# Optimization experiments

Hardware: AMD Instinct MI355X
Metric: run time of the kernel (lower is better)

## Reference

```python
import jax, jax.numpy as jnp
import numpy as np

B, R, T, D = 16, 1024, 512, 1024
H = 1024  # hidden_dim

def setup_inputs() -> dict:
    key = jax.random.key(0)
    ks = jax.random.split(key, 8)
    s_in = 1.0 / np.sqrt(D)
    s_comb = 1.0 / np.sqrt(3 * D)
    return {
        "region_feats": jax.random.normal(ks[0], (B, R, D), jnp.float32),
        "query_embs": jax.random.normal(ks[1], (B, T, D), jnp.float32),
        "Wr": jax.random.normal(ks[2], (D, H), jnp.float32) * s_in,
        "br": jnp.zeros((H,), jnp.float32),
        "Wq": jax.random.normal(ks[3], (D, H), jnp.float32) * s_in,
        "bq": jnp.zeros((H,), jnp.float32),
        "Ws": jax.random.normal(ks[4], (3 * D, 1), jnp.float32) * s_comb,
        "bs": jnp.zeros((1,), jnp.float32),
    }

def reference(region_feats, query_embs, Wr, br, Wq, bq, Ws, bs):
    # Dense projections
    R_proj = region_feats @ Wr + br            # [B,R,H]
    Q_proj = query_embs @ Wq + bq              # [B,T,H]
    # Unscaled cross-attention scores
    scores = jnp.einsum('brd,btd->brt', R_proj, Q_proj)  # [B,R,T]
    attn = jax.nn.softmax(scores, axis=-1)
    # Attend over RAW query embeddings (as in source)
    attended = jnp.einsum('brt,btd->brd', attn, query_embs)  # [B,R,D]
    combined = jnp.concatenate(
        [region_feats, attended, region_feats * attended], axis=-1)  # [B,R,3D]
    out = combined @ Ws + bs                    # [B,R,1]
    return jnp.squeeze(out, axis=-1)            # [B,R]
```

## Files before the change

### kernel.cpp

```cpp
#include <hip/hip_runtime.h>


#define BD 16
#define RD 1024
#define TD 512
#define DD 1024
#define BR (BD * RD)

typedef _Float16 half8 __attribute__((ext_vector_type(8)));
typedef _Float16 half4 __attribute__((ext_vector_type(4)));
typedef float floatx4 __attribute__((ext_vector_type(4)));

__device__ __forceinline__ float wave_sum(float v) {
#pragma unroll
  for (int off = 32; off > 0; off >>= 1) v += __shfl_down(v, off);
  return v;
}

template <bool FUSED>
__global__ __launch_bounds__(512, 4) void gemm_pipe(
    const _Float16* __restrict__ A, const _Float16* __restrict__ B0,
    const _Float16* __restrict__ B1, _Float16* __restrict__ C,
    float* __restrict__ Ms, float* __restrict__ Ls, float* __restrict__ Hs,
    const float* __restrict__ cvec, const _Float16* __restrict__ wsh,
    int N, int K, long sA, long sB, long sC, int remap) {
  constexpr int TT = FUSED ? 3 : 2;
  __shared__ __align__(16) _Float16 lds[2 * TT * 4096];
  __shared__ __align__(16) _Float16 wlds[FUSED ? 2048 : 16];

  const int lin = blockIdx.x + gridDim.x * (blockIdx.y + gridDim.y * blockIdx.z);
  int b, mt, nt;
  if (remap == 2) {
    const int s = lin & 7, u = lin >> 3;
    b = 2 * s + (u >> 5);
    const int t = u & 31;
    mt = t >> 2; nt = t & 3;
  } else if (remap == 1) {
    const int s = lin & 7, u = lin >> 3;
    b = 0;
    mt = s * 8 + (u >> 3); nt = u & 7;
  } else {
    b = blockIdx.z; mt = blockIdx.y; nt = blockIdx.x;
  }
  const int m0 = mt * 128, n0 = nt * 128;
  A += (long)b * sA;
  B0 += (long)b * sB;
  if (FUSED) B1 += (long)b * sB;

  const int tid = threadIdx.x, lane = tid & 63, w = tid >> 6;
  const int wr = w >> 1, wc = w & 1;

  const int lrow = lane >> 2;
  const int slot = lane & 3;
  const int scol = (slot ^ ((lrow >> 1) & 3)) * 8;
  const int srow = 16 * w + lrow;
  const _Float16* gA = A + (long)(m0 + srow) * K + scol;
  const _Float16* gP = B0 + (long)(n0 + srow) * K + scol;
  const _Float16* gQ = FUSED ? B1 + (long)(n0 + srow) * K + scol : nullptr;
  const int wofs = srow * 32 + slot * 8;

  if (FUSED && tid < 256) *(int4*)&wlds[tid * 8] = *(const int4*)&wsh[tid * 8];

  const int NK = K / 32;
  int4 pA, pP, pQ;
  pA = *(const int4*)gA;
  pP = *(const int4*)gP;
  if (FUSED) pQ = *(const int4*)gQ;
  *(int4*)&lds[wofs] = pA;
  *(int4*)&lds[4096 + wofs] = pP;
  if (FUSED) *(int4*)&lds[8192 + wofs] = pQ;
  if (NK > 1) {
    pA = *(const int4*)(gA + 32);
    pP = *(const int4*)(gP + 32);
    if (FUSED) pQ = *(const int4*)(gQ + 32);
  }
  __syncthreads();

  floatx4 accS[2][4] = {};
  floatx4 accH[2][4] = {};
  const int fr = lane & 15, g = lane >> 4;
  const int fs = (g ^ ((fr >> 1) & 3)) * 8;

  for (int kt = 0; kt < NK; ++kt) {
    const int cur = (kt & 1) * TT * 4096;
    const int nxt = ((kt + 1) & 1) * TT * 4096;
    if (kt + 1 < NK) {
      *(int4*)&lds[nxt + wofs] = pA;
      *(int4*)&lds[nxt + 4096 + wofs] = pP;
      if (FUSED) *(int4*)&lds[nxt + 8192 + wofs] = pQ;
    }
    if (kt + 2 < NK) {
      const long go = (long)(kt + 2) * 32;
      pA = *(const int4*)(gA + go);
      pP = *(const int4*)(gP + go);
      if (FUSED) pQ = *(const int4*)(gQ + go);
    }
    half8 af[2], bp[4], bq[4], w1f, w2f;
#pragma unroll
    for (int i = 0; i < 2; ++i)
      af[i] = *(const half8*)&lds[cur + (32 * wr + 16 * i + fr) * 32 + fs];
#pragma unroll
    for (int j = 0; j < 4; ++j)
      bp[j] = *(const half8*)&lds[cur + 4096 + (64 * wc + 16 * j + fr) * 32 + fs];
    if (FUSED) {
#pragma unroll
      for (int j = 0; j < 4; ++j)
        bq[j] = *(const half8*)&lds[cur + 8192 + (64 * wc + 16 * j + fr) * 32 + fs];
      w1f = *(const half8*)&wlds[kt * 32 + g * 8];
      w2f = *(const half8*)&wlds[1024 + kt * 32 + g * 8];
    }
#pragma unroll
    for (int i = 0; i < 2; ++i)
#pragma unroll
      for (int j = 0; j < 4; ++j)
        accS[i][j] = __builtin_amdgcn_mfma_f32_16x16x32_f16(af[i], bp[j], accS[i][j], 0, 0, 0);
    if (FUSED) {
#pragma unroll
      for (int i = 0; i < 2; ++i) af[i] = w1f + af[i] * w2f;
#pragma unroll
      for (int i = 0; i < 2; ++i)
#pragma unroll
        for (int j = 0; j < 4; ++j)
          accH[i][j] = __builtin_amdgcn_mfma_f32_16x16x32_f16(af[i], bq[j], accH[i][j], 0, 0, 0);
    }
    __syncthreads();
  }

  const int cr = g * 4, cc = fr;
  if (!FUSED) {
    _Float16* Cw = C + (long)b * sC;
#pragma unroll
    for (int i = 0; i < 2; ++i)
#pragma unroll
      for (int r = 0; r < 4; ++r)
#pragma unroll
        for (int j = 0; j < 4; ++j)
          Cw[(long)(m0 + 32 * wr + 16 * i + cr + r) * N + n0 + 64 * wc + 16 * j + cc] =
              (_Float16)accS[i][j][r];
  } else {
    float cv[4];
#pragma unroll
    for (int j = 0; j < 4; ++j)
      cv[j] = cvec[(long)b * TD + n0 + 64 * wc + 16 * j + cc];
    const int chunk = nt * 2 + wc;
    const long rowBase = (long)b * RD + m0 + 32 * wr + cr;
#pragma unroll
    for (int i = 0; i < 2; ++i) {
#pragma unroll
      for (int r = 0; r < 4; ++r) {
        float mx = -1e30f;
#pragma unroll
        for (int j = 0; j < 4; ++j) mx = fmaxf(mx, accS[i][j][r] + cv[j]);
        mx = fmaxf(mx, __shfl_xor(mx, 1));
        mx = fmaxf(mx, __shfl_xor(mx, 2));
        mx = fmaxf(mx, __shfl_xor(mx, 4));
        mx = fmaxf(mx, __shfl_xor(mx, 8));
        float l = 0.f, hs = 0.f;
#pragma unroll
        for (int j = 0; j < 4; ++j) {
          const float e = __expf(accS[i][j][r] + cv[j] - mx);
          l += e;
          hs += e * accH[i][j][r];
        }
        l += __shfl_xor(l, 1); hs += __shfl_xor(hs, 1);
        l += __shfl_xor(l, 2); hs += __shfl_xor(hs, 2);
        l += __shfl_xor(l, 4); hs += __shfl_xor(hs, 4);
        l += __shfl_xor(l, 8); hs += __shfl_xor(hs, 8);
        if (cc == 0) {
          const long idx = (long)chunk * BR + rowBase + 16 * i + r;
          Ms[idx] = mx;
          Ls[idx] = l;
          Hs[idx] = hs;
        }
      }
    }
  }
}

__global__ __launch_bounds__(256) void combine(
    const float* __restrict__ Ms, const float* __restrict__ Ls,
    const float* __restrict__ Hs, const float* __restrict__ rdvec,
    const float* __restrict__ bs, float* __restrict__ out) {
  const int row = blockIdx.x * 256 + threadIdx.x;
  float mv[8];
  float gm = -1e30f;
#pragma unroll
  for (int c = 0; c < 8; ++c) {
    mv[c] = Ms[(long)c * BR + row];
    gm = fmaxf(gm, mv[c]);
  }
  float L = 0.f, HS = 0.f;
#pragma unroll
  for (int c = 0; c < 8; ++c) {
    const float s = __expf(mv[c] - gm);
    L += Ls[(long)c * BR + row] * s;
    HS += Hs[(long)c * BR + row] * s;
  }
  out[row] = HS / L + rdvec[row] + bs[0];
}

__global__ __launch_bounds__(256) void prep(
    const float* __restrict__ Wr, const float* __restrict__ Wq,
    const float* __restrict__ Ws, const float* __restrict__ br,
    _Float16* __restrict__ Wr16, _Float16* __restrict__ Wq16,
    _Float16* __restrict__ Ws16, float* __restrict__ wqbr) {
  const int blk = blockIdx.x, tid = threadIdx.x;
  if (blk < 2050) {
    const float* src;
    _Float16* dst;
    long i;
    if (blk < 1024) { src = Wr; dst = Wr16; i = (long)blk * 1024 + tid * 4; }
    else if (blk < 2048) { src = Wq; dst = Wq16; i = (long)(blk - 1024) * 1024 + tid * 4; }
    else { src = Ws + DD; dst = Ws16; i = (long)(blk - 2048) * 1024 + tid * 4; }
    const float4 v = *(const float4*)&src[i];
    half4 h = {(_Float16)v.x, (_Float16)v.y, (_Float16)v.z, (_Float16)v.w};
    *(half4*)&dst[i] = h;
  } else {
    const int row = (blk - 2050) * 4 + (tid >> 6);
    const int lane = tid & 63;
    const float* x = Wq + (long)row * DD;
    float s = 0.f;
    for (int k = lane; k < DD; k += 64) s += x[k] * br[k];
    s = wave_sum(s);
    if (lane == 0) wqbr[row] = s;
  }
}

__global__ __launch_bounds__(256) void conv_region(
    const float* __restrict__ region, const float* __restrict__ Ws,
    _Float16* __restrict__ r16, float* __restrict__ rdvec) {
  const long row = blockIdx.x;
  const int tid = threadIdx.x, lane = tid & 63, wid = tid >> 6;
  const long i = row * DD + tid * 4;
  const float4 v = *(const float4*)&region[i];
  half4 h = {(_Float16)v.x, (_Float16)v.y, (_Float16)v.z, (_Float16)v.w};
  *(half4*)&r16[i] = h;
  const float4 w0 = *(const float4*)&Ws[tid * 4];
  float rd = v.x * w0.x + v.y * w0.y + v.z * w0.z + v.w * w0.w;
  rd = wave_sum(rd);
  __shared__ float sm[4];
  if (lane == 0) sm[wid] = rd;
  __syncthreads();
  if (tid == 0) rdvec[row] = sm[0] + sm[1] + sm[2] + sm[3];
}

__global__ __launch_bounds__(256) void conv_query(
    const float* __restrict__ query, const float* __restrict__ wqbr,
    _Float16* __restrict__ q16, float* __restrict__ cvec) {
  const long row = blockIdx.x;
  const int tid = threadIdx.x, lane = tid & 63, wid = tid >> 6;
  const long i = row * DD + tid * 4;
  const float4 v = *(const float4*)&query[i];
  half4 h = {(_Float16)v.x, (_Float16)v.y, (_Float16)v.z, (_Float16)v.w};
  *(half4*)&q16[i] = h;
  const float4 w = *(const float4*)&wqbr[tid * 4];
  float c = v.x * w.x + v.y * w.y + v.z * w.z + v.w * w.w;
  c = wave_sum(c);
  __shared__ float sm[4];
  if (lane == 0) sm[wid] = c;
  __syncthreads();
  if (tid == 0) cvec[row] = sm[0] + sm[1] + sm[2] + sm[3];
}

extern "C" void kernel_launch(void* const* d_in, const int* in_sizes, int n_in,
                              void* d_out, int out_size, void* d_ws, size_t ws_size,
                              hipStream_t stream) {
  const float* region = (const float*)d_in[0];
  const float* query  = (const float*)d_in[1];
  const float* Wr     = (const float*)d_in[2];
  const float* br     = (const float*)d_in[3];
  const float* Wq     = (const float*)d_in[4];
  const float* Ws     = (const float*)d_in[6];
  const float* bs     = (const float*)d_in[7];
  float* out = (float*)d_out;

  char* p = (char*)d_ws;
  _Float16* region16 = (_Float16*)p;
  _Float16* query16  = (_Float16*)(p + (32u << 20));
  _Float16* Qp       = (_Float16*)(p + (48u << 20));
  _Float16* Wr16     = (_Float16*)(p + (64u << 20));
  _Float16* Wq16     = (_Float16*)(p + (66u << 20));
  _Float16* M2       = (_Float16*)(p + (68u << 20));
  _Float16* Ws16     = (_Float16*)(p + (70u << 20));
  float*    wqbr     = (float*)(p + (70u << 20) + 65536);
  float*    cvec     = wqbr + 1024;
  float*    rdvec    = cvec + BD * TD;
  float*    Ms       = (float*)(p + (72u << 20));
  float*    Ls       = Ms + 8 * BR;
  float*    Hs       = Ls + 8 * BR;

  prep<<<dim3(2306), 256, 0, stream>>>(Wr, Wq, Ws, br, Wr16, Wq16, Ws16, wqbr);
  conv_region<<<dim3(BD * RD), 256, 0, stream>>>(region, Ws, region16, rdvec);
  conv_query<<<dim3(BD * TD), 256, 0, stream>>>(query, wqbr, query16, cvec);

  gemm_pipe<false><<<dim3(8, 8, 1), 512, 0, stream>>>(
      Wr16, Wq16, nullptr, M2, nullptr, nullptr, nullptr, nullptr, nullptr,
      DD, DD, 0, 0, 0, 0);
  gemm_pipe<false><<<dim3(8, 64, 1), 512, 0, stream>>>(
      query16, M2, nullptr, Qp, nullptr, nullptr, nullptr, nullptr, nullptr,
      DD, DD, 0, 0, 0, 1);
  gemm_pipe<true><<<dim3(TD / 128, RD / 128, BD), 512, 0, stream>>>(
      region16, Qp, query16, nullptr, Ms, Ls, Hs, cvec, Ws16,
      TD, DD, (long)RD * DD, (long)TD * DD, 0, 2);
  combine<<<dim3(BR / 256), 256, 0, stream>>>(Ms, Ls, Hs, rdvec, bs, out);
}
```

Measured before the change: 229.3 us.

## Use 4-wave blocks with 64x64 per-wave tiles in pipelined GEMM

The GEMM kernel drops from 8 waves of 512 threads to 4 waves of 256 threads per 128x128 tile. Each wave now computes a 64x64 sub-tile with 4x4 MFMA fragments instead of 32x64, and each thread loads two rows per operand into LDS. The aim is more MFMA work per LDS fragment read and fewer waves contending per tile. The cost is doubled accumulator registers, which is heavy in the fused path with both S and H accumulators, so occupancy drops and spills are possible.

```diff
diff --git a/kernel.cpp b/kernel.cpp
--- a/kernel.cpp
+++ b/kernel.cpp
@@ -18,7 +18,7 @@
 }
 
 template <bool FUSED>
-__global__ __launch_bounds__(512, 4) void gemm_pipe(
+__global__ __launch_bounds__(256, 2) void gemm_pipe(
     const _Float16* __restrict__ A, const _Float16* __restrict__ B0,
     const _Float16* __restrict__ B1, _Float16* __restrict__ C,
     float* __restrict__ Ms, float* __restrict__ Ls, float* __restrict__ Hs,
@@ -50,34 +50,48 @@
   const int tid = threadIdx.x, lane = tid & 63, w = tid >> 6;
   const int wr = w >> 1, wc = w & 1;
 
-  const int lrow = lane >> 2;
-  const int slot = lane & 3;
-  const int scol = (slot ^ ((lrow >> 1) & 3)) * 8;
-  const int srow = 16 * w + lrow;
-  const _Float16* gA = A + (long)(m0 + srow) * K + scol;
-  const _Float16* gP = B0 + (long)(n0 + srow) * K + scol;
-  const _Float16* gQ = FUSED ? B1 + (long)(n0 + srow) * K + scol : nullptr;
+  const int srow = tid >> 2;
+  const int slot = tid & 3;
+  const int scol = (slot ^ ((srow >> 1) & 3)) * 8;
+  const long offA = (long)(m0 + srow) * K + scol;
+  const long offB = (long)(n0 + srow) * K + scol;
+  const long rstep = (long)64 * K;
   const int wofs = srow * 32 + slot * 8;
 
-  if (FUSED && tid < 256) *(int4*)&wlds[tid * 8] = *(const int4*)&wsh[tid * 8];
+  if (FUSED) *(int4*)&wlds[tid * 8] = *(const int4*)&wsh[tid * 8];
 
   const int NK = K / 32;
-  int4 pA, pP, pQ;
-  pA = *(const int4*)gA;
-  pP = *(const int4*)gP;
-  if (FUSED) pQ = *(const int4*)gQ;
-  *(int4*)&lds[wofs] = pA;
-  *(int4*)&lds[4096 + wofs] = pP;
-  if (FUSED) *(int4*)&lds[8192 + wofs] = pQ;
+  int4 pA0, pA1, pP0, pP1, pQ0, pQ1;
+  pA0 = *(const int4*)(A + offA);
+  pA1 = *(const int4*)(A + offA + rstep);
+  pP0 = *(const int4*)(B0 + offB);
+  pP1 = *(const int4*)(B0 + offB + rstep);
+  if (FUSED) {
+    pQ0 = *(const int4*)(B1 + offB);
+    pQ1 = *(const int4*)(B1 + offB + rstep);
+  }
+  *(int4*)&lds[wofs] = pA0;
+  *(int4*)&lds[wofs + 2048] = pA1;
+  *(int4*)&lds[4096 + wofs] = pP0;
+  *(int4*)&lds[4096 + wofs + 2048] = pP1;
+  if (FUSED) {
+    *(int4*)&lds[8192 + wofs] = pQ0;
+    *(int4*)&lds[8192 + wofs + 2048] = pQ1;
+  }
   if (NK > 1) {
-    pA = *(const int4*)(gA + 32);
-    pP = *(const int4*)(gP + 32);
-    if (FUSED) pQ = *(const int4*)(gQ + 32);
+    pA0 = *(const int4*)(A + offA + 32);
+    pA1 = *(const int4*)(A + offA + rstep + 32);
+    pP0 = *(const int4*)(B0 + offB + 32);
+    pP1 = *(const int4*)(B0 + offB + rstep + 32);
+    if (FUSED) {
+      pQ0 = *(const int4*)(B1 + offB + 32);
+      pQ1 = *(const int4*)(B1 + offB + rstep + 32);
+    }
   }
   __syncthreads();
 
-  floatx4 accS[2][4] = {};
-  floatx4 accH[2][4] = {};
+  floatx4 accS[4][4] = {};
+  floatx4 accH[4][4] = {};
   const int fr = lane & 15, g = lane >> 4;
   const int fs = (g ^ ((fr >> 1) & 3)) * 8;
 
@@ -85,20 +99,30 @@
     const int cur = (kt & 1) * TT * 4096;
     const int nxt = ((kt + 1) & 1) * TT * 4096;
     if (kt + 1 < NK) {
-      *(int4*)&lds[nxt + wofs] = pA;
-      *(int4*)&lds[nxt + 4096 + wofs] = pP;
-      if (FUSED) *(int4*)&lds[nxt + 8192 + wofs] = pQ;
+      *(int4*)&lds[nxt + wofs] = pA0;
+      *(int4*)&lds[nxt + wofs + 2048] = pA1;
+      *(int4*)&lds[nxt + 4096 + wofs] = pP0;
+      *(int4*)&lds[nxt + 4096 + wofs + 2048] = pP1;
+      if (FUSED) {
+        *(int4*)&lds[nxt + 8192 + wofs] = pQ0;
+        *(int4*)&lds[nxt + 8192 + wofs + 2048] = pQ1;
+      }
     }
     if (kt + 2 < NK) {
       const long go = (long)(kt + 2) * 32;
-      pA = *(const int4*)(gA + go);
-      pP = *(const int4*)(gP + go);
-      if (FUSED) pQ = *(const int4*)(gQ + go);
-    }
-    half8 af[2], bp[4], bq[4], w1f, w2f;
-#pragma unroll
-    for (int i = 0; i < 2; ++i)
-      af[i] = *(const half8*)&lds[cur + (32 * wr + 16 * i + fr) * 32 + fs];
+      pA0 = *(const int4*)(A + offA + go);
+      pA1 = *(const int4*)(A + offA + rstep + go);
+      pP0 = *(const int4*)(B0 + offB + go);
+      pP1 = *(const int4*)(B0 + offB + rstep + go);
+      if (FUSED) {
+        pQ0 = *(const int4*)(B1 + offB + go);
+        pQ1 = *(const int4*)(B1 + offB + rstep + go);
+      }
+    }
+    half8 af[4], bp[4], bq[4], w1f, w2f;
+#pragma unroll
+    for (int i = 0; i < 4; ++i)
+      af[i] = *(const half8*)&lds[cur + (64 * wr + 16 * i + fr) * 32 + fs];
 #pragma unroll
     for (int j = 0; j < 4; ++j)
       bp[j] = *(const half8*)&lds[cur + 4096 + (64 * wc + 16 * j + fr) * 32 + fs];
@@ -110,15 +134,15 @@
       w2f = *(const half8*)&wlds[1024 + kt * 32 + g * 8];
     }
 #pragma unroll
-    for (int i = 0; i < 2; ++i)
+    for (int i = 0; i < 4; ++i)
 #pragma unroll
       for (int j = 0; j < 4; ++j)
         accS[i][j] = __builtin_amdgcn_mfma_f32_16x16x32_f16(af[i], bp[j], accS[i][j], 0, 0, 0);
     if (FUSED) {
 #pragma unroll
-      for (int i = 0; i < 2; ++i) af[i] = w1f + af[i] * w2f;
-#pragma unroll
-      for (int i = 0; i < 2; ++i)
+      for (int i = 0; i < 4; ++i) af[i] = w1f + af[i] * w2f;
+#pragma unroll
+      for (int i = 0; i < 4; ++i)
 #pragma unroll
         for (int j = 0; j < 4; ++j)
           accH[i][j] = __builtin_amdgcn_mfma_f32_16x16x32_f16(af[i], bq[j], accH[i][j], 0, 0, 0);
@@ -130,12 +154,12 @@
   if (!FUSED) {
     _Float16* Cw = C + (long)b * sC;
 #pragma unroll
-    for (int i = 0; i < 2; ++i)
+    for (int i = 0; i < 4; ++i)
 #pragma unroll
       for (int r = 0; r < 4; ++r)
 #pragma unroll
         for (int j = 0; j < 4; ++j)
-          Cw[(long)(m0 + 32 * wr + 16 * i + cr + r) * N + n0 + 64 * wc + 16 * j + cc] =
+          Cw[(long)(m0 + 64 * wr + 16 * i + cr + r) * N + n0 + 64 * wc + 16 * j + cc] =
               (_Float16)accS[i][j][r];
   } else {
     float cv[4];
@@ -143,9 +167,9 @@
     for (int j = 0; j < 4; ++j)
       cv[j] = cvec[(long)b * TD + n0 + 64 * wc + 16 * j + cc];
     const int chunk = nt * 2 + wc;
-    const long rowBase = (long)b * RD + m0 + 32 * wr + cr;
-#pragma unroll
-    for (int i = 0; i < 2; ++i) {
+    const long rowBase = (long)b * RD + m0 + 64 * wr + cr;
+#pragma unroll
+    for (int i = 0; i < 4; ++i) {
 #pragma unroll
       for (int r = 0; r < 4; ++r) {
         float mx = -1e30f;
@@ -293,13 +317,13 @@
   conv_region<<<dim3(BD * RD), 256, 0, stream>>>(region, Ws, region16, rdvec);
   conv_query<<<dim3(BD * TD), 256, 0, stream>>>(query, wqbr, query16, cvec);
 
-  gemm_pipe<false><<<dim3(8, 8, 1), 512, 0, stream>>>(
+  gemm_pipe<false><<<dim3(8, 8, 1), 256, 0, stream>>>(
       Wr16, Wq16, nullptr, M2, nullptr, nullptr, nullptr, nullptr, nullptr,
       DD, DD, 0, 0, 0, 0);
-  gemm_pipe<false><<<dim3(8, 64, 1), 512, 0, stream>>>(
+  gemm_pipe<false><<<dim3(8, 64, 1), 256, 0, stream>>>(
       query16, M2, nullptr, Qp, nullptr, nullptr, nullptr, nullptr, nullptr,
       DD, DD, 0, 0, 0, 1);
-  gemm_pipe<true><<<dim3(TD / 128, RD / 128, BD), 512, 0, stream>>>(
+  gemm_pipe<true><<<dim3(TD / 128, RD / 128, BD), 256, 0, stream>>>(
       region16, Qp, query16, nullptr, Ms, Ls, Hs, cvec, Ws16,
       TD, DD, (long)RD * DD, (long)TD * DD, 0, 2);
   combine<<<dim3(BR / 256), 256, 0, stream>>>(Ms, Ls, Hs, rdvec, bs, out);
```

Result: slower. 236.8 us (+3.3%).
